# Performance work log

Hardware: AMD Instinct MI355X
Metric: run time of the kernel (lower is better)

Reference implementation:

```python
import jax, jax.numpy as jnp
import numpy as np

B, T, H, FS, K = 64, 2048, 256, 256, 3
WIN = 16  # sliding-window history length of textEmb


def flex_sigmoid(x, a, b, c, d):
    # a*b*x / (1 + (b*|x|)^c)^(1/c) + d*x   (paramC != 0 branch)
    return a * b * x / jnp.power(1.0 + jnp.power(b * jnp.abs(x), c), 1.0 / c) + d * x


def layer_norm(x, g, b, eps=1e-5):
    mu = jnp.mean(x, axis=-1, keepdims=True)
    var = jnp.var(x, axis=-1, keepdims=True)
    return (x - mu) * jax.lax.rsqrt(var + eps) * g + b


def conv1d(x, w, b, pad):
    # x: [B,T,C], w: [O,I,K] -> [B,T,O]
    y = jax.lax.conv_general_dilated(
        x.transpose(0, 2, 1), w, window_strides=(1,), padding=[(pad, pad)],
        dimension_numbers=('NCH', 'OIH', 'NCH'))
    return y.transpose(0, 2, 1) + b


def setup_inputs() -> dict:
    key = jax.random.key(0)
    ks = jax.random.split(key, 16)
    s1 = 1.0 / np.sqrt((H + WIN) * K)
    s2 = 1.0 / np.sqrt(FS * K)
    sl = 1.0 / np.sqrt(FS)
    return {
        'encoder_output': jax.random.normal(ks[0], (B, T, H), jnp.float32),
        'mask': jax.random.randint(ks[1], (B, T), 0, 2).astype(bool),
        'textEmb': jax.random.normal(ks[2], (B, T), jnp.float32),
        'w1': jax.random.uniform(ks[3], (FS, H + WIN, K), jnp.float32, -s1, s1),
        'b1': jnp.zeros((FS,), jnp.float32),
        'fa1': jnp.array([2.35], jnp.float32), 'fb1': jnp.array([1.35], jnp.float32),
        'fc1': jnp.array([2.35], jnp.float32), 'fd1': jnp.array([0.05], jnp.float32),
        'g1': jnp.ones((FS,), jnp.float32), 'be1': jnp.zeros((FS,), jnp.float32),
        'w2': jax.random.uniform(ks[4], (FS, FS, K), jnp.float32, -s2, s2),
        'b2': jnp.zeros((FS,), jnp.float32),
        'fa2': jnp.array([2.3], jnp.float32), 'fb2': jnp.array([1.4], jnp.float32),
        'fc2': jnp.array([2.4], jnp.float32), 'fd2': jnp.array([0.02], jnp.float32),
        'g2': jnp.ones((FS,), jnp.float32), 'be2': jnp.zeros((FS,), jnp.float32),
        'wl': jax.random.uniform(ks[5], (FS, 1), jnp.float32, -sl, sl),
        'bl': jnp.zeros((1,), jnp.float32),
    }


def reference(encoder_output, mask, textEmb, w1, b1, fa1, fb1, fc1, fd1, g1, be1,
              w2, b2, fa2, fb2, fc2, fd2, g2, be2, wl, bl):
    Tn = encoder_output.shape[1]
    # vectorized sliding-window gather: full_textEmb[i,j,k] = textEmb[i,j-k] or -1
    idx = jnp.arange(Tn)[:, None] - jnp.arange(WIN)[None, :]  # [T,16]
    gathered = textEmb[:, jnp.clip(idx, 0, None)]             # [B,T,16]
    full_textEmb = jnp.where(idx >= 0, gathered, -1.0)
    out = jnp.concatenate([encoder_output, full_textEmb], axis=2)  # [B,T,H+16]
    # conv stack (dropout is identity in eval)
    out = conv1d(out, w1, b1, (K - 1) // 2)
    out = flex_sigmoid(out, fa1, fb1, fc1, fd1)
    out = layer_norm(out, g1, be1)
    out = conv1d(out, w2, b2, 1)
    out = flex_sigmoid(out, fa2, fb2, fc2, fd2)
    out = layer_norm(out, g2, be2)
    out = out @ wl + bl            # [B,T,1]
    out = out[..., 0]
    return jnp.where(mask, 0.0, out)
```

## Files before the change

kernel.cpp:

```cpp
#include <hip/hip_runtime.h>
#include <hip/hip_bf16.h>


#define BB 64
#define TT 2048
#define HH 256
#define FSZ 256
#define KW 3
#define WIN 16
#define CIN1 272
#define TILE_T 64

#define NCS1 9
#define NK1 27
#define CP1B 640
#define NCS2 8
#define NK2 24
#define CP2B 512

typedef __attribute__((ext_vector_type(8))) short bf16x8;
typedef __attribute__((ext_vector_type(4))) float f32x4;

__device__ __forceinline__ unsigned short f2bf(float f) {
  unsigned int u = __float_as_uint(f);
  unsigned int r = (u + 0x7fffu + ((u >> 16) & 1u)) >> 16;
  return (unsigned short)r;
}

__device__ __forceinline__ float flexsig(float x, float a, float b, float c,
                                         float invc, float d) {
  float ax = fabsf(x);
  float t = __expf(c * __logf(b * ax));
  float den = __expf(invc * __logf(1.0f + t));
  return a * b * x / den + d * x;
}

__global__ void detect_mask_kernel(const unsigned int* __restrict__ m,
                                   int* __restrict__ flag) {
  __shared__ int s_big, s_flt;
  if (threadIdx.x == 0) { s_big = 0; s_flt = 0; }
  __syncthreads();
  int big = 0, flt = 0;
  const int nwords = (BB * TT) / 4;
  for (int i = threadIdx.x; i < nwords; i += blockDim.x) {
    unsigned int w = m[i];
    if (w == 0x3F800000u) flt = 1;
    else if (w > 1u) big = 1;
  }
  if (big) atomicOr(&s_big, 1);
  if (flt) atomicOr(&s_flt, 1);
  __syncthreads();
  if (threadIdx.x == 0) flag[0] = s_flt ? 2 : (s_big ? 1 : 0);
}

__device__ __forceinline__ bool read_mask(const void* maskp, size_t i, int fl) {
  if (fl == 0) return ((const int*)maskp)[i] != 0;
  if (fl == 1) return ((const unsigned char*)maskp)[i] != 0;
  return ((const float*)maskp)[i] != 0.0f;
}

__global__ void repack_mfma(const float* __restrict__ w1, const float* __restrict__ w2,
                            unsigned short* __restrict__ wb1,
                            unsigned short* __restrict__ wb2) {
  int idx = blockIdx.x * blockDim.x + threadIdx.x;
  const int n1 = NK1 * 16 * 64 * 8;
  if (idx < n1) {
    int j = idx & 7, lane = (idx >> 3) & 63, nf = (idx >> 9) & 15, rest = idx >> 13;
    int s = rest / NCS1, cs = rest - s * NCS1;
    int c = cs * 32 + (lane >> 4) * 8 + j;
    int f = nf * 16 + (lane & 15);
    float v = (c < CIN1) ? w1[(f * CIN1 + c) * KW + s] : 0.0f;
    wb1[idx] = f2bf(v);
  }
  const int n2 = NK2 * 16 * 64 * 8;
  if (idx < n2) {
    int j = idx & 7, lane = (idx >> 3) & 63, nf = (idx >> 9) & 15, rest = idx >> 13;
    int s = rest >> 3, cs = rest & 7;
    int c = cs * 32 + (lane >> 4) * 8 + j;
    int f = nf * 16 + (lane & 15);
    wb2[idx] = f2bf(w2[(f * FSZ + c) * KW + s]);
  }
}

__global__ __launch_bounds__(256, 2)
void k1_mfma(const float* __restrict__ enc, const float* __restrict__ temb,
             const bf16x8* __restrict__ wb1, const float* __restrict__ b1g,
             const float* __restrict__ fa, const float* __restrict__ fb,
             const float* __restrict__ fc, const float* __restrict__ fd,
             const float* __restrict__ g1, const float* __restrict__ be1,
             unsigned short* __restrict__ y1, int b0) {
  __shared__ __attribute__((aligned(16))) char sA[66 * CP1B];
  __shared__ float2 lnbuf[64][4];
  __shared__ float mu_s[64], rs_s[64];
  __shared__ float gs[256], bs[256], bias_s[256];

  const int tid = threadIdx.x;
  const int b = b0 + blockIdx.y;
  const int by = blockIdx.y;
  const int t0 = blockIdx.x * TILE_T;
  const int lane = tid & 63;
  const int wid = tid >> 6;
  const int l15 = lane & 15;
  const int lhi = lane >> 4;

  gs[tid] = g1[tid]; bs[tid] = be1[tid]; bias_s[tid] = b1g[tid];

  for (int i = tid; i < 66 * 36; i += 256) {
    int row = i / 36;
    int g = i - row * 36;
    int t = t0 + row - 1;
    bool tv = (t >= 0) && (t < TT);
    float x[8];
    if (g < 32) {
      if (tv) {
        const float4* p = reinterpret_cast<const float4*>(&enc[((size_t)b * TT + t) * HH + g * 8]);
        float4 v0 = p[0], v1 = p[1];
        x[0] = v0.x; x[1] = v0.y; x[2] = v0.z; x[3] = v0.w;
        x[4] = v1.x; x[5] = v1.y; x[6] = v1.z; x[7] = v1.w;
      } else {
#pragma unroll
        for (int j = 0; j < 8; ++j) x[j] = 0.0f;
      }
    } else if (g < 34) {
      int w0 = (g - 32) * 8;
#pragma unroll
      for (int j = 0; j < 8; ++j) {
        int w = w0 + j;
        float v = 0.0f;
        if (tv) v = (t - w >= 0) ? temb[(size_t)b * TT + t - w] : -1.0f;
        x[j] = v;
      }
    } else {
#pragma unroll
      for (int j = 0; j < 8; ++j) x[j] = 0.0f;
    }
    bf16x8 pk;
#pragma unroll
    for (int j = 0; j < 8; ++j) pk[j] = (short)f2bf(x[j]);
    int byte = row * CP1B + ((g * 16) ^ ((row & 7) << 4));
    *reinterpret_cast<bf16x8*>(&sA[byte]) = pk;
  }
  __syncthreads();

  f32x4 acc[4][4];
#pragma unroll
  for (int mf = 0; mf < 4; ++mf)
#pragma unroll
    for (int nf = 0; nf < 4; ++nf) acc[mf][nf] = (f32x4)(0.0f);

  auto loadA = [&](int ks, bf16x8 aF[4]) {
    int s = (ks >= 2 * NCS1) ? 2 : ((ks >= NCS1) ? 1 : 0);
    int cs = ks - s * NCS1;
    int row0 = l15 + s;
    int cb = (cs * 64 + lhi * 16) ^ ((row0 & 7) << 4);
    int base = row0 * CP1B + cb;
#pragma unroll
    for (int mf = 0; mf < 4; ++mf)
      aF[mf] = *reinterpret_cast<const bf16x8*>(&sA[base + mf * (16 * CP1B)]);
  };
  auto loadB = [&](int ks, bf16x8 bF[4]) {
    const bf16x8* p = wb1 + (size_t)(ks * 16 + wid * 4) * 64 + lane;
#pragma unroll
    for (int nf = 0; nf < 4; ++nf) bF[nf] = p[nf * 64];
  };
  auto mm = [&](bf16x8 aF[4], bf16x8 bF[4]) {
#pragma unroll
    for (int mf = 0; mf < 4; ++mf)
#pragma unroll
      for (int nf = 0; nf < 4; ++nf)
        acc[mf][nf] = __builtin_amdgcn_mfma_f32_16x16x32_bf16(aF[mf], bF[nf], acc[mf][nf], 0, 0, 0);
  };

  bf16x8 aP[4], bP[4], aQ[4], bQ[4];
  loadA(0, aP); loadB(0, bP);
  int ks = 0;
  for (; ks + 1 < NK1; ks += 2) {
    loadA(ks + 1, aQ); loadB(ks + 1, bQ);
    mm(aP, bP);
    if (ks + 2 < NK1) { loadA(ks + 2, aP); loadB(ks + 2, bP); }
    mm(aQ, bQ);
  }
  if (ks < NK1) mm(aP, bP);

  const float fA = fa[0], fB = fb[0], fC = fc[0], fD = fd[0];
  const float inv_c = 1.0f / fC;
#pragma unroll
  for (int mf = 0; mf < 4; ++mf)
#pragma unroll
    for (int nf = 0; nf < 4; ++nf) {
      int col = wid * 64 + nf * 16 + l15;
      float bias = bias_s[col];
#pragma unroll
      for (int r = 0; r < 4; ++r)
        acc[mf][nf][r] = flexsig(acc[mf][nf][r] + bias, fA, fB, fC, inv_c, fD);
    }

#pragma unroll
  for (int mf = 0; mf < 4; ++mf)
#pragma unroll
    for (int r = 0; r < 4; ++r) {
      float s = 0.0f, q = 0.0f;
#pragma unroll
      for (int nf = 0; nf < 4; ++nf) {
        float v = acc[mf][nf][r];
        s += v; q += v * v;
      }
      s += __shfl_xor(s, 1); q += __shfl_xor(q, 1);
      s += __shfl_xor(s, 2); q += __shfl_xor(q, 2);
      s += __shfl_xor(s, 4); q += __shfl_xor(q, 4);
      s += __shfl_xor(s, 8); q += __shfl_xor(q, 8);
      if (l15 == 0) lnbuf[mf * 16 + lhi * 4 + r][wid] = make_float2(s, q);
    }
  __syncthreads();
  if (tid < 64) {
    float S = 0.0f, Q = 0.0f;
#pragma unroll
    for (int w = 0; w < 4; ++w) { S += lnbuf[tid][w].x; Q += lnbuf[tid][w].y; }
    float mu = S * (1.0f / 256.0f);
    float var = Q * (1.0f / 256.0f) - mu * mu;
    mu_s[tid] = mu; rs_s[tid] = rsqrtf(var + 1e-5f);
  }
  __syncthreads();

#pragma unroll
  for (int mf = 0; mf < 4; ++mf)
#pragma unroll
    for (int nf = 0; nf < 4; ++nf) {
      int col = wid * 64 + nf * 16 + l15;
      float gg = gs[col], bb = bs[col];
#pragma unroll
      for (int r = 0; r < 4; ++r) {
        int row = mf * 16 + lhi * 4 + r;
        float v = (acc[mf][nf][r] - mu_s[row]) * rs_s[row] * gg + bb;
        int byte = row * 512 + ((col * 2) ^ ((row & 7) << 4));
        *reinterpret_cast<unsigned short*>(&sA[byte]) = f2bf(v);
      }
    }
  __syncthreads();

  for (int i = tid; i < 64 * 32; i += 256) {
    int row = i >> 5, g = i & 31;
    int byte = row * 512 + ((g * 16) ^ ((row & 7) << 4));
    bf16x8 v = *reinterpret_cast<const bf16x8*>(&sA[byte]);
    *reinterpret_cast<bf16x8*>(&y1[((size_t)by * TT + t0 + row) * FSZ + g * 8]) = v;
  }
}

__global__ __launch_bounds__(256, 2)
void k2_mfma(const unsigned short* __restrict__ y1, const bf16x8* __restrict__ wb2,
             const float* __restrict__ b2g,
             const float* __restrict__ fa, const float* __restrict__ fb,
             const float* __restrict__ fc, const float* __restrict__ fd,
             const float* __restrict__ g2, const float* __restrict__ be2,
             const float* __restrict__ wl, const float* __restrict__ bl,
             const void* __restrict__ maskp, const int* __restrict__ flag,
             float* __restrict__ out, int b0) {
  __shared__ __attribute__((aligned(16))) char sA[66 * CP2B];
  __shared__ float2 lnbuf[64][4];
  __shared__ float pbuf[64][4];
  __shared__ float mu_s[64], rs_s[64];
  __shared__ float gs[256], bs[256], bias_s[256], wls[256];

  const int tid = threadIdx.x;
  const int b = b0 + blockIdx.y;
  const int by = blockIdx.y;
  const int t0 = blockIdx.x * TILE_T;
  const int lane = tid & 63;
  const int wid = tid >> 6;
  const int l15 = lane & 15;
  const int lhi = lane >> 4;

  gs[tid] = g2[tid]; bs[tid] = be2[tid]; bias_s[tid] = b2g[tid]; wls[tid] = wl[tid];

  for (int i = tid; i < 66 * 32; i += 256) {
    int row = i >> 5, g = i & 31;
    int t = t0 + row - 1;
    bf16x8 v;
#pragma unroll
    for (int j = 0; j < 8; ++j) v[j] = 0;
    if (t >= 0 && t < TT)
      v = *reinterpret_cast<const bf16x8*>(&y1[((size_t)by * TT + t) * FSZ + g * 8]);
    int byte = row * CP2B + ((g * 16) ^ ((row & 7) << 4));
    *reinterpret_cast<bf16x8*>(&sA[byte]) = v;
  }
  __syncthreads();

  f32x4 acc[4][4];
#pragma unroll
  for (int mf = 0; mf < 4; ++mf)
#pragma unroll
    for (int nf = 0; nf < 4; ++nf) acc[mf][nf] = (f32x4)(0.0f);

  auto loadA = [&](int ks, bf16x8 aF[4]) {
    int s = (ks >= 2 * NCS2) ? 2 : ((ks >= NCS2) ? 1 : 0);
    int cs = ks - s * NCS2;
    int row0 = l15 + s;
    int cb = (cs * 64 + lhi * 16) ^ ((row0 & 7) << 4);
    int base = row0 * CP2B + cb;
#pragma unroll
    for (int mf = 0; mf < 4; ++mf)
      aF[mf] = *reinterpret_cast<const bf16x8*>(&sA[base + mf * (16 * CP2B)]);
  };
  auto loadB = [&](int ks, bf16x8 bF[4]) {
    const bf16x8* p = wb2 + (size_t)(ks * 16 + wid * 4) * 64 + lane;
#pragma unroll
    for (int nf = 0; nf < 4; ++nf) bF[nf] = p[nf * 64];
  };
  auto mm = [&](bf16x8 aF[4], bf16x8 bF[4]) {
#pragma unroll
    for (int mf = 0; mf < 4; ++mf)
#pragma unroll
      for (int nf = 0; nf < 4; ++nf)
        acc[mf][nf] = __builtin_amdgcn_mfma_f32_16x16x32_bf16(aF[mf], bF[nf], acc[mf][nf], 0, 0, 0);
  };

  bf16x8 aP[4], bP[4], aQ[4], bQ[4];
  loadA(0, aP); loadB(0, bP);
  int ks = 0;
  for (; ks + 1 < NK2; ks += 2) {
    loadA(ks + 1, aQ); loadB(ks + 1, bQ);
    mm(aP, bP);
    if (ks + 2 < NK2) { loadA(ks + 2, aP); loadB(ks + 2, bP); }
    mm(aQ, bQ);
  }
  if (ks < NK2) mm(aP, bP);

  const float fA = fa[0], fB = fb[0], fC = fc[0], fD = fd[0];
  const float inv_c = 1.0f / fC;
#pragma unroll
  for (int mf = 0; mf < 4; ++mf)
#pragma unroll
    for (int nf = 0; nf < 4; ++nf) {
      int col = wid * 64 + nf * 16 + l15;
      float bias = bias_s[col];
#pragma unroll
      for (int r = 0; r < 4; ++r)
        acc[mf][nf][r] = flexsig(acc[mf][nf][r] + bias, fA, fB, fC, inv_c, fD);
    }

#pragma unroll
  for (int mf = 0; mf < 4; ++mf)
#pragma unroll
    for (int r = 0; r < 4; ++r) {
      float s = 0.0f, q = 0.0f;
#pragma unroll
      for (int nf = 0; nf < 4; ++nf) {
        float v = acc[mf][nf][r];
        s += v; q += v * v;
      }
      s += __shfl_xor(s, 1); q += __shfl_xor(q, 1);
      s += __shfl_xor(s, 2); q += __shfl_xor(q, 2);
      s += __shfl_xor(s, 4); q += __shfl_xor(q, 4);
      s += __shfl_xor(s, 8); q += __shfl_xor(q, 8);
      if (l15 == 0) lnbuf[mf * 16 + lhi * 4 + r][wid] = make_float2(s, q);
    }
  __syncthreads();
  if (tid < 64) {
    float S = 0.0f, Q = 0.0f;
#pragma unroll
    for (int w = 0; w < 4; ++w) { S += lnbuf[tid][w].x; Q += lnbuf[tid][w].y; }
    float mu = S * (1.0f / 256.0f);
    float var = Q * (1.0f / 256.0f) - mu * mu;
    mu_s[tid] = mu; rs_s[tid] = rsqrtf(var + 1e-5f);
  }
  __syncthreads();

  float p[4][4];
#pragma unroll
  for (int mf = 0; mf < 4; ++mf)
#pragma unroll
    for (int r = 0; r < 4; ++r) p[mf][r] = 0.0f;
#pragma unroll
  for (int mf = 0; mf < 4; ++mf)
#pragma unroll
    for (int nf = 0; nf < 4; ++nf) {
      int col = wid * 64 + nf * 16 + l15;
      float gg = gs[col], bb = bs[col], ww = wls[col];
#pragma unroll
      for (int r = 0; r < 4; ++r) {
        int row = mf * 16 + lhi * 4 + r;
        float v = (acc[mf][nf][r] - mu_s[row]) * rs_s[row] * gg + bb;
        p[mf][r] += v * ww;
      }
    }
#pragma unroll
  for (int mf = 0; mf < 4; ++mf)
#pragma unroll
    for (int r = 0; r < 4; ++r) {
      float v = p[mf][r];
      v += __shfl_xor(v, 1);
      v += __shfl_xor(v, 2);
      v += __shfl_xor(v, 4);
      v += __shfl_xor(v, 8);
      if (l15 == 0) pbuf[mf * 16 + lhi * 4 + r][wid] = v;
    }
  __syncthreads();
  if (tid < 64) {
    float s = pbuf[tid][0] + pbuf[tid][1] + pbuf[tid][2] + pbuf[tid][3] + bl[0];
    int t = t0 + tid;
    size_t mi = (size_t)b * TT + t;
    bool m = read_mask(maskp, mi, flag[0]);
    out[mi] = m ? 0.0f : s;
  }
}

extern "C" void kernel_launch(void* const* d_in, const int* in_sizes, int n_in,
                              void* d_out, int out_size, void* d_ws, size_t ws_size,
                              hipStream_t stream) {
  const float* enc  = (const float*)d_in[0];
  const void*  maskp= d_in[1];
  const float* temb = (const float*)d_in[2];
  const float* w1   = (const float*)d_in[3];
  const float* b1   = (const float*)d_in[4];
  const float* fa1  = (const float*)d_in[5];
  const float* fb1  = (const float*)d_in[6];
  const float* fc1  = (const float*)d_in[7];
  const float* fd1  = (const float*)d_in[8];
  const float* g1   = (const float*)d_in[9];
  const float* be1  = (const float*)d_in[10];
  const float* w2   = (const float*)d_in[11];
  const float* b2   = (const float*)d_in[12];
  const float* fa2  = (const float*)d_in[13];
  const float* fb2  = (const float*)d_in[14];
  const float* fc2  = (const float*)d_in[15];
  const float* fd2  = (const float*)d_in[16];
  const float* g2   = (const float*)d_in[17];
  const float* be2  = (const float*)d_in[18];
  const float* wl   = (const float*)d_in[19];
  const float* bl   = (const float*)d_in[20];
  float* out = (float*)d_out;

  char* ws = (char*)d_ws;
  const size_t wb1_bytes = (size_t)NK1 * 16 * 64 * 8 * 2;
  const size_t wb2_bytes = (size_t)NK2 * 16 * 64 * 8 * 2;
  unsigned short* wb1 = (unsigned short*)ws;
  unsigned short* wb2 = (unsigned short*)(ws + wb1_bytes);
  int* flag = (int*)(ws + wb1_bytes + wb2_bytes);
  unsigned short* y1 = (unsigned short*)(ws + wb1_bytes + wb2_bytes + 256);

  const size_t head = wb1_bytes + wb2_bytes + 256;
  const size_t perB = (size_t)TT * FSZ * 2;
  size_t avail = (ws_size > head) ? (ws_size - head) : 0;
  size_t cb = avail / perB;
  int chunkB = (cb >= BB) ? BB : (int)cb;
  if (chunkB < 1) chunkB = 1;

  detect_mask_kernel<<<1, 256, 0, stream>>>((const unsigned int*)maskp, flag);
  {
    int n = NK1 * 16 * 64 * 8;
    repack_mfma<<<(n + 255) / 256, 256, 0, stream>>>(w1, w2, wb1, wb2);
  }

  for (int b0 = 0; b0 < BB; b0 += chunkB) {
    int nb = (BB - b0 < chunkB) ? (BB - b0) : chunkB;
    dim3 grid(TT / TILE_T, nb);
    k1_mfma<<<grid, 256, 0, stream>>>(enc, temb, (const bf16x8*)wb1, b1,
                                      fa1, fb1, fc1, fd1, g1, be1, y1, b0);
    k2_mfma<<<grid, 256, 0, stream>>>(y1, (const bf16x8*)wb2, b2,
                                      fa2, fb2, fc2, fd2, g2, be2, wl, bl,
                                      maskp, flag, out, b0);
  }
}
```

Before: 484.2 us.

## Halve time tile, raise occupancy, and fuse mask detection into weight repack

Halves the time tile from 64 to 32 rows and raises launch bounds to 4 blocks per CU, cutting per-block LDS and registers so more waves can be resident. The single-block mask-type detection scan is merged into the weight repack kernel and spread over 64 blocks using atomics on a memset flag. Per-channel parameters are now read straight from global memory instead of being staged in shared memory, and the k-loop is fully unrolled. In exchange, halo rows are re-read more often relative to useful rows (34/32 instead of 66/64), B-fragment weight traffic per output row doubles, and the extra memset adds a launch.

Measured after the change: 415.1 us. 1.17x faster.

```diff
diff --git a/kernel.cpp b/kernel.cpp
--- a/kernel.cpp
+++ b/kernel.cpp
@@ -9,7 +9,8 @@
 #define KW 3
 #define WIN 16
 #define CIN1 272
-#define TILE_T 64
+#define TILE_T 32
+#define ROWS (TILE_T + 2)
 
 #define NCS1 9
 #define NK1 27
@@ -35,64 +36,60 @@
   return a * b * x / den + d * x;
 }
 
-__global__ void detect_mask_kernel(const unsigned int* __restrict__ m,
-                                   int* __restrict__ flag) {
-  __shared__ int s_big, s_flt;
-  if (threadIdx.x == 0) { s_big = 0; s_flt = 0; }
-  __syncthreads();
-  int big = 0, flt = 0;
-  const int nwords = (BB * TT) / 4;
-  for (int i = threadIdx.x; i < nwords; i += blockDim.x) {
-    unsigned int w = m[i];
-    if (w == 0x3F800000u) flt = 1;
-    else if (w > 1u) big = 1;
-  }
-  if (big) atomicOr(&s_big, 1);
-  if (flt) atomicOr(&s_flt, 1);
-  __syncthreads();
-  if (threadIdx.x == 0) flag[0] = s_flt ? 2 : (s_big ? 1 : 0);
-}
-
 __device__ __forceinline__ bool read_mask(const void* maskp, size_t i, int fl) {
   if (fl == 0) return ((const int*)maskp)[i] != 0;
   if (fl == 1) return ((const unsigned char*)maskp)[i] != 0;
   return ((const float*)maskp)[i] != 0.0f;
 }
 
-__global__ void repack_mfma(const float* __restrict__ w1, const float* __restrict__ w2,
+__global__ void prep_kernel(const float* __restrict__ w1, const float* __restrict__ w2,
                             unsigned short* __restrict__ wb1,
-                            unsigned short* __restrict__ wb2) {
-  int idx = blockIdx.x * blockDim.x + threadIdx.x;
-  const int n1 = NK1 * 16 * 64 * 8;
-  if (idx < n1) {
-    int j = idx & 7, lane = (idx >> 3) & 63, nf = (idx >> 9) & 15, rest = idx >> 13;
-    int s = rest / NCS1, cs = rest - s * NCS1;
-    int c = cs * 32 + (lane >> 4) * 8 + j;
-    int f = nf * 16 + (lane & 15);
-    float v = (c < CIN1) ? w1[(f * CIN1 + c) * KW + s] : 0.0f;
-    wb1[idx] = f2bf(v);
-  }
-  const int n2 = NK2 * 16 * 64 * 8;
-  if (idx < n2) {
-    int j = idx & 7, lane = (idx >> 3) & 63, nf = (idx >> 9) & 15, rest = idx >> 13;
-    int s = rest >> 3, cs = rest & 7;
-    int c = cs * 32 + (lane >> 4) * 8 + j;
-    int f = nf * 16 + (lane & 15);
-    wb2[idx] = f2bf(w2[(f * FSZ + c) * KW + s]);
-  }
-}
-
-__global__ __launch_bounds__(256, 2)
+                            unsigned short* __restrict__ wb2,
+                            const unsigned int* __restrict__ m,
+                            int* __restrict__ flag) {
+  const int bid = blockIdx.x;
+  if (bid < 864) {
+    int idx = bid * 256 + threadIdx.x;
+    {
+      int j = idx & 7, lane = (idx >> 3) & 63, nf = (idx >> 9) & 15, rest = idx >> 13;
+      int s = rest / NCS1, cs = rest - s * NCS1;
+      int c = cs * 32 + (lane >> 4) * 8 + j;
+      int f = nf * 16 + (lane & 15);
+      float v = (c < CIN1) ? w1[(f * CIN1 + c) * KW + s] : 0.0f;
+      wb1[idx] = f2bf(v);
+    }
+    const int n2 = NK2 * 16 * 64 * 8;
+    if (idx < n2) {
+      int j = idx & 7, lane = (idx >> 3) & 63, nf = (idx >> 9) & 15, rest = idx >> 13;
+      int s = rest >> 3, cs = rest & 7;
+      int c = cs * 32 + (lane >> 4) * 8 + j;
+      int f = nf * 16 + (lane & 15);
+      wb2[idx] = f2bf(w2[(f * FSZ + c) * KW + s]);
+    }
+  } else {
+    int t = (bid - 864) * 256 + threadIdx.x;
+    int big = 0, flt = 0;
+    const int nwords = (BB * TT) / 4;
+    for (int i = t; i < nwords; i += 64 * 256) {
+      unsigned int w = m[i];
+      if (w == 0x3F800000u) flt = 1;
+      else if (w > 1u) big = 1;
+    }
+    if (__any(big) && (threadIdx.x & 63) == 0) atomicOr(&flag[1], 1);
+    if (__any(flt) && (threadIdx.x & 63) == 0) atomicOr(&flag[2], 1);
+  }
+}
+
+__global__ __launch_bounds__(256, 4)
 void k1_mfma(const float* __restrict__ enc, const float* __restrict__ temb,
              const bf16x8* __restrict__ wb1, const float* __restrict__ b1g,
              const float* __restrict__ fa, const float* __restrict__ fb,
              const float* __restrict__ fc, const float* __restrict__ fd,
              const float* __restrict__ g1, const float* __restrict__ be1,
              unsigned short* __restrict__ y1, int b0) {
-  __shared__ __attribute__((aligned(16))) char sA[66 * CP1B];
-  __shared__ float2 lnbuf[64][4];
-  __shared__ float mu_s[64], rs_s[64];
-  __shared__ float gs[256], bs[256], bias_s[256];
+  __shared__ __attribute__((aligned(16))) char sA[ROWS * CP1B];
+  __shared__ float2 lnbuf[TILE_T][4];
+  __shared__ float mu_s[TILE_T], rs_s[TILE_T];
 
   const int tid = threadIdx.x;
   const int b = b0 + blockIdx.y;
@@ -103,9 +100,7 @@
   const int l15 = lane & 15;
   const int lhi = lane >> 4;
 
-  gs[tid] = g1[tid]; bs[tid] = be1[tid]; bias_s[tid] = b1g[tid];
-
-  for (int i = tid; i < 66 * 36; i += 256) {
+  for (int i = tid; i < ROWS * 36; i += 256) {
     int row = i / 36;
     int g = i - row * 36;
     int t = t0 + row - 1;
@@ -142,20 +137,20 @@
   }
   __syncthreads();
 
-  f32x4 acc[4][4];
-#pragma unroll
-  for (int mf = 0; mf < 4; ++mf)
+  f32x4 acc[2][4];
+#pragma unroll
+  for (int mf = 0; mf < 2; ++mf)
 #pragma unroll
     for (int nf = 0; nf < 4; ++nf) acc[mf][nf] = (f32x4)(0.0f);
 
-  auto loadA = [&](int ks, bf16x8 aF[4]) {
+  auto loadA = [&](int ks, bf16x8 aF[2]) {
     int s = (ks >= 2 * NCS1) ? 2 : ((ks >= NCS1) ? 1 : 0);
     int cs = ks - s * NCS1;
     int row0 = l15 + s;
     int cb = (cs * 64 + lhi * 16) ^ ((row0 & 7) << 4);
     int base = row0 * CP1B + cb;
 #pragma unroll
-    for (int mf = 0; mf < 4; ++mf)
+    for (int mf = 0; mf < 2; ++mf)
       aF[mf] = *reinterpret_cast<const bf16x8*>(&sA[base + mf * (16 * CP1B)]);
   };
   auto loadB = [&](int ks, bf16x8 bF[4]) {
@@ -163,40 +158,40 @@
 #pragma unroll
     for (int nf = 0; nf < 4; ++nf) bF[nf] = p[nf * 64];
   };
-  auto mm = [&](bf16x8 aF[4], bf16x8 bF[4]) {
-#pragma unroll
-    for (int mf = 0; mf < 4; ++mf)
+  auto mm = [&](bf16x8 aF[2], bf16x8 bF[4]) {
+#pragma unroll
+    for (int mf = 0; mf < 2; ++mf)
 #pragma unroll
       for (int nf = 0; nf < 4; ++nf)
         acc[mf][nf] = __builtin_amdgcn_mfma_f32_16x16x32_bf16(aF[mf], bF[nf], acc[mf][nf], 0, 0, 0);
   };
 
-  bf16x8 aP[4], bP[4], aQ[4], bQ[4];
+  bf16x8 aP[2], bP[4], aQ[2], bQ[4];
   loadA(0, aP); loadB(0, bP);
-  int ks = 0;
-  for (; ks + 1 < NK1; ks += 2) {
+#pragma unroll
+  for (int ks = 0; ks + 1 < NK1; ks += 2) {
     loadA(ks + 1, aQ); loadB(ks + 1, bQ);
     mm(aP, bP);
     if (ks + 2 < NK1) { loadA(ks + 2, aP); loadB(ks + 2, bP); }
     mm(aQ, bQ);
   }
-  if (ks < NK1) mm(aP, bP);
+  if (NK1 & 1) mm(aP, bP);
 
   const float fA = fa[0], fB = fb[0], fC = fc[0], fD = fd[0];
   const float inv_c = 1.0f / fC;
 #pragma unroll
-  for (int mf = 0; mf < 4; ++mf)
+  for (int mf = 0; mf < 2; ++mf)
 #pragma unroll
     for (int nf = 0; nf < 4; ++nf) {
       int col = wid * 64 + nf * 16 + l15;
-      float bias = bias_s[col];
+      float bias = b1g[col];
 #pragma unroll
       for (int r = 0; r < 4; ++r)
         acc[mf][nf][r] = flexsig(acc[mf][nf][r] + bias, fA, fB, fC, inv_c, fD);
     }
 
 #pragma unroll
-  for (int mf = 0; mf < 4; ++mf)
+  for (int mf = 0; mf < 2; ++mf)
 #pragma unroll
     for (int r = 0; r < 4; ++r) {
       float s = 0.0f, q = 0.0f;
@@ -212,7 +207,7 @@
       if (l15 == 0) lnbuf[mf * 16 + lhi * 4 + r][wid] = make_float2(s, q);
     }
   __syncthreads();
-  if (tid < 64) {
+  if (tid < TILE_T) {
     float S = 0.0f, Q = 0.0f;
 #pragma unroll
     for (int w = 0; w < 4; ++w) { S += lnbuf[tid][w].x; Q += lnbuf[tid][w].y; }
@@ -223,11 +218,11 @@
   __syncthreads();
 
 #pragma unroll
-  for (int mf = 0; mf < 4; ++mf)
+  for (int mf = 0; mf < 2; ++mf)
 #pragma unroll
     for (int nf = 0; nf < 4; ++nf) {
       int col = wid * 64 + nf * 16 + l15;
-      float gg = gs[col], bb = bs[col];
+      float gg = g1[col], bb = be1[col];
 #pragma unroll
       for (int r = 0; r < 4; ++r) {
         int row = mf * 16 + lhi * 4 + r;
@@ -238,7 +233,7 @@
     }
   __syncthreads();
 
-  for (int i = tid; i < 64 * 32; i += 256) {
+  for (int i = tid; i < TILE_T * 32; i += 256) {
     int row = i >> 5, g = i & 31;
     int byte = row * 512 + ((g * 16) ^ ((row & 7) << 4));
     bf16x8 v = *reinterpret_cast<const bf16x8*>(&sA[byte]);
@@ -246,20 +241,19 @@
   }
 }
 
-__global__ __launch_bounds__(256, 2)
+__global__ __launch_bounds__(256, 4)
 void k2_mfma(const unsigned short* __restrict__ y1, const bf16x8* __restrict__ wb2,
              const float* __restrict__ b2g,
              const float* __restrict__ fa, const float* __restrict__ fb,
              const float* __restrict__ fc, const float* __restrict__ fd,
              const float* __restrict__ g2, const float* __restrict__ be2,
              const float* __restrict__ wl, const float* __restrict__ bl,
-             const void* __restrict__ maskp, const int* __restrict__ flag,
+             const void* __restrict__ maskp, const int* __restrict__ flagp,
              float* __restrict__ out, int b0) {
-  __shared__ __attribute__((aligned(16))) char sA[66 * CP2B];
-  __shared__ float2 lnbuf[64][4];
-  __shared__ float pbuf[64][4];
-  __shared__ float mu_s[64], rs_s[64];
-  __shared__ float gs[256], bs[256], bias_s[256], wls[256];
+  __shared__ __attribute__((aligned(16))) char sA[ROWS * CP2B];
+  __shared__ float2 lnbuf[TILE_T][4];
+  __shared__ float pbuf[TILE_T][4];
+  __shared__ float mu_s[TILE_T], rs_s[TILE_T];
 
   const int tid = threadIdx.x;
   const int b = b0 + blockIdx.y;
@@ -270,9 +264,7 @@
   const int l15 = lane & 15;
   const int lhi = lane >> 4;
 
-  gs[tid] = g2[tid]; bs[tid] = be2[tid]; bias_s[tid] = b2g[tid]; wls[tid] = wl[tid];
-
-  for (int i = tid; i < 66 * 32; i += 256) {
+  for (int i = tid; i < ROWS * 32; i += 256) {
     int row = i >> 5, g = i & 31;
     int t = t0 + row - 1;
     bf16x8 v;
@@ -285,20 +277,20 @@
   }
   __syncthreads();
 
-  f32x4 acc[4][4];
-#pragma unroll
-  for (int mf = 0; mf < 4; ++mf)
+  f32x4 acc[2][4];
+#pragma unroll
+  for (int mf = 0; mf < 2; ++mf)
 #pragma unroll
     for (int nf = 0; nf < 4; ++nf) acc[mf][nf] = (f32x4)(0.0f);
 
-  auto loadA = [&](int ks, bf16x8 aF[4]) {
+  auto loadA = [&](int ks, bf16x8 aF[2]) {
     int s = (ks >= 2 * NCS2) ? 2 : ((ks >= NCS2) ? 1 : 0);
     int cs = ks - s * NCS2;
     int row0 = l15 + s;
     int cb = (cs * 64 + lhi * 16) ^ ((row0 & 7) << 4);
     int base = row0 * CP2B + cb;
 #pragma unroll
-    for (int mf = 0; mf < 4; ++mf)
+    for (int mf = 0; mf < 2; ++mf)
       aF[mf] = *reinterpret_cast<const bf16x8*>(&sA[base + mf * (16 * CP2B)]);
   };
   auto loadB = [&](int ks, bf16x8 bF[4]) {
@@ -306,40 +298,40 @@
 #pragma unroll
     for (int nf = 0; nf < 4; ++nf) bF[nf] = p[nf * 64];
   };
-  auto mm = [&](bf16x8 aF[4], bf16x8 bF[4]) {
-#pragma unroll
-    for (int mf = 0; mf < 4; ++mf)
+  auto mm = [&](bf16x8 aF[2], bf16x8 bF[4]) {
+#pragma unroll
+    for (int mf = 0; mf < 2; ++mf)
 #pragma unroll
       for (int nf = 0; nf < 4; ++nf)
         acc[mf][nf] = __builtin_amdgcn_mfma_f32_16x16x32_bf16(aF[mf], bF[nf], acc[mf][nf], 0, 0, 0);
   };
 
-  bf16x8 aP[4], bP[4], aQ[4], bQ[4];
+  bf16x8 aP[2], bP[4], aQ[2], bQ[4];
   loadA(0, aP); loadB(0, bP);
-  int ks = 0;
-  for (; ks + 1 < NK2; ks += 2) {
+#pragma unroll
+  for (int ks = 0; ks + 1 < NK2; ks += 2) {
     loadA(ks + 1, aQ); loadB(ks + 1, bQ);
     mm(aP, bP);
     if (ks + 2 < NK2) { loadA(ks + 2, aP); loadB(ks + 2, bP); }
     mm(aQ, bQ);
   }
-  if (ks < NK2) mm(aP, bP);
+  if (NK2 & 1) mm(aP, bP);
 
   const float fA = fa[0], fB = fb[0], fC = fc[0], fD = fd[0];
   const float inv_c = 1.0f / fC;
 #pragma unroll
-  for (int mf = 0; mf < 4; ++mf)
+  for (int mf = 0; mf < 2; ++mf)
 #pragma unroll
     for (int nf = 0; nf < 4; ++nf) {
       int col = wid * 64 + nf * 16 + l15;
-      float bias = bias_s[col];
+      float bias = b2g[col];
 #pragma unroll
       for (int r = 0; r < 4; ++r)
         acc[mf][nf][r] = flexsig(acc[mf][nf][r] + bias, fA, fB, fC, inv_c, fD);
     }
 
 #pragma unroll
-  for (int mf = 0; mf < 4; ++mf)
+  for (int mf = 0; mf < 2; ++mf)
 #pragma unroll
     for (int r = 0; r < 4; ++r) {
       float s = 0.0f, q = 0.0f;
@@ -355,7 +347,7 @@
       if (l15 == 0) lnbuf[mf * 16 + lhi * 4 + r][wid] = make_float2(s, q);
     }
   __syncthreads();
-  if (tid < 64) {
+  if (tid < TILE_T) {
     float S = 0.0f, Q = 0.0f;
 #pragma unroll
     for (int w = 0; w < 4; ++w) { S += lnbuf[tid][w].x; Q += lnbuf[tid][w].y; }
@@ -365,17 +357,17 @@
   }
   __syncthreads();
 
-  float p[4][4];
-#pragma unroll
-  for (int mf = 0; mf < 4; ++mf)
+  float p[2][4];
+#pragma unroll
+  for (int mf = 0; mf < 2; ++mf)
 #pragma unroll
     for (int r = 0; r < 4; ++r) p[mf][r] = 0.0f;
 #pragma unroll
-  for (int mf = 0; mf < 4; ++mf)
+  for (int mf = 0; mf < 2; ++mf)
 #pragma unroll
     for (int nf = 0; nf < 4; ++nf) {
       int col = wid * 64 + nf * 16 + l15;
-      float gg = gs[col], bb = bs[col], ww = wls[col];
+      float gg = g2[col], bb = be2[col], ww = wl[col];
 #pragma unroll
       for (int r = 0; r < 4; ++r) {
         int row = mf * 16 + lhi * 4 + r;
@@ -384,7 +376,7 @@
       }
     }
 #pragma unroll
-  for (int mf = 0; mf < 4; ++mf)
+  for (int mf = 0; mf < 2; ++mf)
 #pragma unroll
     for (int r = 0; r < 4; ++r) {
       float v = p[mf][r];
@@ -395,11 +387,12 @@
       if (l15 == 0) pbuf[mf * 16 + lhi * 4 + r][wid] = v;
     }
   __syncthreads();
-  if (tid < 64) {
+  if (tid < TILE_T) {
     float s = pbuf[tid][0] + pbuf[tid][1] + pbuf[tid][2] + pbuf[tid][3] + bl[0];
     int t = t0 + tid;
     size_t mi = (size_t)b * TT + t;
-    bool m = read_mask(maskp, mi, flag[0]);
+    int fl = flagp[2] ? 2 : (flagp[1] ? 1 : 0);
+    bool m = read_mask(maskp, mi, fl);
     out[mi] = m ? 0.0f : s;
   }
 }
@@ -445,11 +438,9 @@
   int chunkB = (cb >= BB) ? BB : (int)cb;
   if (chunkB < 1) chunkB = 1;
 
-  detect_mask_kernel<<<1, 256, 0, stream>>>((const unsigned int*)maskp, flag);
-  {
-    int n = NK1 * 16 * 64 * 8;
-    repack_mfma<<<(n + 255) / 256, 256, 0, stream>>>(w1, w2, wb1, wb2);
-  }
+  hipMemsetAsync(flag, 0, 16, stream);
+  prep_kernel<<<928, 256, 0, stream>>>(w1, w2, wb1, wb2,
+                                       (const unsigned int*)maskp, flag);
 
   for (int b0 = 0; b0 < BB; b0 += chunkB) {
     int nb = (BB - b0 < chunkB) ? (BB - b0) : chunkB;
```
